# Kernel tuning notes

Hardware: AMD Instinct MI355X
Metric: run time of the kernel (lower is better)

The kernel has to match this reference:

```python
import jax, jax.numpy as jnp
import numpy as np

S_DIM, I_DIM, O_DIM = 1024, 2048, 1024
TOTAL = S_DIM + I_DIM + O_DIM  # 4096
INPUT_DIM, NUM_CLASSES, BATCH = 2048, 1000, 256


def setup_inputs() -> dict:
    key = jax.random.key(0)
    ks = jax.random.split(key, 6)
    x = jax.random.normal(ks[0], (BATCH, INPUT_DIM), dtype=jnp.float32)
    W = jax.random.normal(ks[1], (TOTAL, TOTAL), dtype=jnp.float32) * 0.02
    # torch Linear: weight [out, in], bias [out]
    in_w = jax.random.normal(ks[2], (S_DIM, INPUT_DIM), dtype=jnp.float32) * (1.0 / np.sqrt(INPUT_DIM))
    in_b = jax.random.normal(ks[3], (S_DIM,), dtype=jnp.float32) * 0.01
    out_w = jax.random.normal(ks[4], (NUM_CLASSES, O_DIM), dtype=jnp.float32) * (1.0 / np.sqrt(O_DIM))
    out_b = jax.random.normal(ks[5], (NUM_CLASSES,), dtype=jnp.float32) * 0.01
    return {"x": x, "W": W, "in_w": in_w, "in_b": in_b, "out_w": out_w, "out_b": out_b, "time_steps": 10}


def reference(x, W, in_w, in_b, out_w, out_b, time_steps):
    B = x.shape[0]
    S, I, O = S_DIM, I_DIM, O_DIM
    # slice effective W into 9 sub-blocks (use_lora=False -> W_eff = W)
    W_ss, W_sr, W_so = W[:S, :S], W[:S, S:S + I], W[:S, S + I:]
    W_rs, W_rr, W_ro = W[S:S + I, :S], W[S:S + I, S:S + I], W[S:S + I, S + I:]
    W_os, W_or, W_oo = W[S + I:, :S], W[S + I:, S:S + I], W[S + I:, S + I:]

    E = x @ in_w.T + in_b  # [B, S]
    gate = (jnp.arange(time_steps) % 5 == 0).astype(x.dtype)  # E injected when t%5==0

    init = (jnp.zeros((B, S), x.dtype), jnp.zeros((B, I), x.dtype), jnp.zeros((B, O), x.dtype))

    def step(carry, g):
        Ss, Is, Os = carry
        S_next = jax.nn.relu(Ss @ W_ss + g * E + Is @ W_rs + Os @ W_os)
        I_next = jax.nn.relu(Is @ W_rr + Ss @ W_sr + Os @ W_or)
        O_next = jax.nn.relu(Os @ W_oo + Is @ W_ro + Ss @ W_so)
        return (S_next, I_next, O_next), None

    (Ss, Is, Os), _ = jax.lax.scan(step, init, gate)
    return Os @ out_w.T + out_b  # [B, num_classes]
```

## Files before the change

### kernel.cpp

```cpp
#include <hip/hip_runtime.h>


typedef __bf16 bf16x8 __attribute__((ext_vector_type(8)));
typedef float  f32x16 __attribute__((ext_vector_type(16)));

#define TOTAL   4096
#define BATCH   256
#define INDIM   2048
#define SDIM    1024
#define NCLS    1000

__device__ inline f32x16 zero16() {
    f32x16 v;
#pragma unroll
    for (int i = 0; i < 16; ++i) v[i] = 0.f;
    return v;
}

__global__ __launch_bounds__(256) void k_transW_swz(const float* __restrict__ W,
                                                    __bf16* __restrict__ WT) {
    __shared__ float t[64][65];
    const int n0 = blockIdx.x * 64;
    const int k0 = blockIdx.y * 64;
    const int x = threadIdx.x & 63;
    const int y = threadIdx.x >> 6;
#pragma unroll
    for (int r = y; r < 64; r += 4)
        t[r][x] = W[(size_t)(k0 + r) * TOTAL + (n0 + x)];
    __syncthreads();
#pragma unroll
    for (int s = threadIdx.x; s < 512; s += 256) {
        const int frag = s >> 6;
        const int lane = s & 63;
        const int lrt = frag >> 2;
        const int lkc = frag & 3;
        const int r_local = lrt * 32 + (lane & 31);
        const int c_local = lkc * 16 + (lane >> 5) * 8;
        alignas(16) __bf16 v[8];
#pragma unroll
        for (int j = 0; j < 8; ++j) v[j] = (__bf16)t[c_local + j][r_local];
        const size_t fragG = (size_t)((n0 >> 5) + lrt) * (TOTAL / 16) + ((k0 >> 4) + lkc);
        *(ulonglong2*)(WT + fragG * 512 + lane * 8) = *(const ulonglong2*)v;
    }
}

__global__ __launch_bounds__(256) void k_swz(const float* __restrict__ in,
                                             __bf16* __restrict__ out,
                                             int C, int Rvalid) {
    const int t = blockIdx.x * blockDim.x + threadIdx.x;
    const int lane = t & 63;
    const int frag = t >> 6;
    const int kcN = C >> 4;
    const int rt = frag / kcN;
    const int kc = frag - rt * kcN;
    const int r = rt * 32 + (lane & 31);
    const int c = kc * 16 + (lane >> 5) * 8;
    alignas(16) __bf16 v[8];
    if (r < Rvalid) {
        const float* p = in + (size_t)r * C + c;
#pragma unroll
        for (int j = 0; j < 8; ++j) v[j] = (__bf16)p[j];
    } else {
#pragma unroll
        for (int j = 0; j < 8; ++j) v[j] = (__bf16)0.f;
    }
    *(ulonglong2*)(out + (size_t)t * 8) = *(const ulonglong2*)v;
}

__global__ __launch_bounds__(512, 4) void k_gemm_E(const __bf16* __restrict__ xt,
                                                   const __bf16* __restrict__ iwt,
                                                   const float* __restrict__ in_b,
                                                   float* __restrict__ E,
                                                   __bf16* __restrict__ h0) {
    __shared__ float red[8][1024];
    const int wave = threadIdx.x >> 6;
    const int lane = threadIdx.x & 63;
    const int mt = blockIdx.x >> 5;
    const int nt = blockIdx.x & 31;
    const int m0 = mt * 32, n0 = nt * 32;
    const int kc0 = wave * 16;
    const bf16x8* Ap = (const bf16x8*)xt  + ((size_t)mt * (INDIM / 16) + kc0) * 64 + lane;
    const bf16x8* Bp = (const bf16x8*)iwt + ((size_t)nt * (INDIM / 16) + kc0) * 64 + lane;
    f32x16 acc = zero16();
#pragma unroll 4
    for (int i = 0; i < 16; ++i) {
        bf16x8 a = Ap[i * 64];
        bf16x8 b = Bp[i * 64];
        acc = __builtin_amdgcn_mfma_f32_32x32x16_bf16(a, b, acc, 0, 0, 0);
    }
#pragma unroll
    for (int r = 0; r < 16; ++r) {
        int row = (r & 3) + 8 * (r >> 2) + 4 * (lane >> 5);
        red[wave][row * 32 + (lane & 31)] = acc[r];
    }
    __syncthreads();
    const int e0 = threadIdx.x * 2;
    float sx = 0.f, sy = 0.f;
#pragma unroll
    for (int w = 0; w < 8; ++w) {
        float2 v = *(const float2*)&red[w][e0];
        sx += v.x; sy += v.y;
    }
    const int row = e0 >> 5, col = e0 & 31;
    const int m = m0 + row, n = n0 + col;
    float v0 = sx + in_b[n], v1 = sy + in_b[n + 1];
    E[m * SDIM + n]     = v0;
    E[m * SDIM + n + 1] = v1;
    __bf16 o[2];
    o[0] = (__bf16)fmaxf(v0, 0.f);
    o[1] = (__bf16)fmaxf(v1, 0.f);
    const size_t frag = (size_t)(m >> 5) * (TOTAL / 16) + (n >> 4);
    const int lh = (m & 31) + 32 * ((n >> 3) & 1);
    *(uint*)(h0 + frag * 512 + lh * 8 + (n & 7)) = *(const uint*)o;
}

__global__ __launch_bounds__(512, 2) void k_step(const __bf16* __restrict__ h,
                                                 const __bf16* __restrict__ WT,
                                                 const float* __restrict__ E,
                                                 const int gate,
                                                 __bf16* __restrict__ hn,
                                                 const int chunks) {
    __shared__ float buf[4][4096];
    const int wave = threadIdx.x >> 6;
    const int lane = threadIdx.x & 63;
    const int mt = blockIdx.x >> 6;
    const int nt = blockIdx.x & 63;
    const int per = chunks >> 3;
    const int kc0 = wave * per;

    const bf16x8* A0 = (const bf16x8*)h  + ((size_t)(mt * 2) * (TOTAL / 16) + kc0) * 64 + lane;
    const bf16x8* A1 = A0 + (size_t)(TOTAL / 16) * 64;
    const bf16x8* B0 = (const bf16x8*)WT + ((size_t)(nt * 2) * (TOTAL / 16) + kc0) * 64 + lane;
    const bf16x8* B1 = B0 + (size_t)(TOTAL / 16) * 64;

    f32x16 ac0 = zero16(), ac1 = zero16(), ac2 = zero16(), ac3 = zero16();
#pragma unroll 4
    for (int i = 0; i < per; ++i) {
        const int off = i * 64;
        bf16x8 a0 = A0[off];
        bf16x8 a1 = A1[off];
        bf16x8 b0 = B0[off];
        bf16x8 b1 = B1[off];
        ac0 = __builtin_amdgcn_mfma_f32_32x32x16_bf16(a0, b0, ac0, 0, 0, 0);
        ac1 = __builtin_amdgcn_mfma_f32_32x32x16_bf16(a0, b1, ac1, 0, 0, 0);
        ac2 = __builtin_amdgcn_mfma_f32_32x32x16_bf16(a1, b0, ac2, 0, 0, 0);
        ac3 = __builtin_amdgcn_mfma_f32_32x32x16_bf16(a1, b1, ac3, 0, 0, 0);
    }

    float* accp[4];
    f32x16 accs[4] = {ac0, ac1, ac2, ac3};
    if (wave >= 4) {
        float* b = buf[wave - 4];
#pragma unroll
        for (int c = 0; c < 4; ++c)
#pragma unroll
            for (int r = 0; r < 16; ++r)
                b[(c * 16 + r) * 64 + lane] = accs[c][r];
    }
    __syncthreads();
    if (wave < 4) {
        float* b = buf[wave];
#pragma unroll
        for (int c = 0; c < 4; ++c)
#pragma unroll
            for (int r = 0; r < 16; ++r) {
                const int idx = (c * 16 + r) * 64 + lane;
                b[idx] += accs[c][r];
            }
    }
    __syncthreads();

    const int t = threadIdx.x;
    const int c = t >> 7;
    const int r = (t >> 3) & 15;
    const int l0 = (t & 7) * 8;
    const int base = (c * 16 + r) * 64 + l0;
    float4 s0 = {0.f, 0.f, 0.f, 0.f}, s1 = {0.f, 0.f, 0.f, 0.f};
#pragma unroll
    for (int w = 0; w < 4; ++w) {
        const float4* p = (const float4*)&buf[w][base];
        float4 v0 = p[0], v1 = p[1];
        s0.x += v0.x; s0.y += v0.y; s0.z += v0.z; s0.w += v0.w;
        s1.x += v1.x; s1.y += v1.y; s1.z += v1.z; s1.w += v1.w;
    }
    float v[8] = {s0.x, s0.y, s0.z, s0.w, s1.x, s1.y, s1.z, s1.w};
    const int ih = c >> 1, jh = c & 1;
    const int row = ih * 32 + (r & 3) + 8 * (r >> 2) + 4 * (l0 >> 5);
    const int col0 = jh * 32 + (l0 & 31);
    const int m = mt * 64 + row;
    const int n0g = nt * 64 + col0;
    if (gate && n0g < SDIM) {
        const float* Ep = E + m * SDIM + n0g;
#pragma unroll
        for (int j = 0; j < 8; ++j) v[j] += Ep[j];
    }
    alignas(16) __bf16 o[8];
#pragma unroll
    for (int j = 0; j < 8; ++j) o[j] = (__bf16)fmaxf(v[j], 0.f);
    const size_t frag = (size_t)(m >> 5) * (TOTAL / 16) + (n0g >> 4);
    const int lh = (m & 31) + 32 * ((n0g >> 3) & 1);
    *(ulonglong2*)(hn + frag * 512 + lh * 8) = *(const ulonglong2*)o;
    (void)accp;
}

__global__ __launch_bounds__(512, 4) void k_out(const __bf16* __restrict__ h,
                                                const __bf16* __restrict__ owt,
                                                const float* __restrict__ out_b,
                                                float* __restrict__ out) {
    __shared__ float red[8][1024];
    const int wave = threadIdx.x >> 6;
    const int lane = threadIdx.x & 63;
    const int mt = blockIdx.x >> 5;
    const int ct = blockIdx.x & 31;
    const int m0 = mt * 32, c0 = ct * 32;
    const int kcA0 = (3072 / 16) + wave * 8;
    const int kcB0 = wave * 8;
    const bf16x8* Ap = (const bf16x8*)h   + ((size_t)mt * (TOTAL / 16) + kcA0) * 64 + lane;
    const bf16x8* Bp = (const bf16x8*)owt + ((size_t)ct * (1024 / 16) + kcB0) * 64 + lane;
    f32x16 acc = zero16();
#pragma unroll
    for (int i = 0; i < 8; ++i) {
        bf16x8 a = Ap[i * 64];
        bf16x8 b = Bp[i * 64];
        acc = __builtin_amdgcn_mfma_f32_32x32x16_bf16(a, b, acc, 0, 0, 0);
    }
#pragma unroll
    for (int r = 0; r < 16; ++r) {
        int row = (r & 3) + 8 * (r >> 2) + 4 * (lane >> 5);
        red[wave][row * 32 + (lane & 31)] = acc[r];
    }
    __syncthreads();
    const int e0 = threadIdx.x * 2;
    float sx = 0.f, sy = 0.f;
#pragma unroll
    for (int w = 0; w < 8; ++w) {
        float2 v = *(const float2*)&red[w][e0];
        sx += v.x; sy += v.y;
    }
    const int row = e0 >> 5, col = e0 & 31;
    const int m = m0 + row;
    const int n = c0 + col;
    if (n < NCLS)     out[m * NCLS + n]     = sx + out_b[n];
    if (n + 1 < NCLS) out[m * NCLS + n + 1] = sy + out_b[n + 1];
}

extern "C" void kernel_launch(void* const* d_in, const int* in_sizes, int n_in,
                              void* d_out, int out_size, void* d_ws, size_t ws_size,
                              hipStream_t stream) {
    const float* x     = (const float*)d_in[0];
    const float* W     = (const float*)d_in[1];
    const float* in_w  = (const float*)d_in[2];
    const float* in_b  = (const float*)d_in[3];
    const float* out_w = (const float*)d_in[4];
    const float* out_b = (const float*)d_in[5];
    float* out = (float*)d_out;

    char* ws = (char*)d_ws;
    __bf16* WT  = (__bf16*)(ws + 0);
    __bf16* XT  = (__bf16*)(ws + 33554432);
    __bf16* IWT = (__bf16*)(ws + 34603008);
    __bf16* OWT = (__bf16*)(ws + 38797312);
    float*  Ebuf= (float*)(ws + 40894464);
    __bf16* H0  = (__bf16*)(ws + 41943040);
    __bf16* H1  = (__bf16*)(ws + 44040192);

    k_transW_swz<<<dim3(64, 64), 256, 0, stream>>>(W, WT);
    k_swz<<<256,  256, 0, stream>>>(x,     XT,  INDIM, BATCH);
    k_swz<<<1024, 256, 0, stream>>>(in_w,  IWT, INDIM, SDIM);
    k_swz<<<512,  256, 0, stream>>>(out_w, OWT, 1024,  NCLS);

    k_gemm_E<<<256, 512, 0, stream>>>(XT, IWT, in_b, Ebuf, H0);

    const __bf16* hs = H0;
    __bf16* hd = H1;
    for (int t = 1; t < 10; ++t) {
        const int chunks = (t == 1) ? (SDIM / 16) : (TOTAL / 16);
        k_step<<<256, 512, 0, stream>>>(hs, WT, Ebuf, (t % 5 == 0) ? 1 : 0, hd, chunks);
        const __bf16* tmp = hs; hs = hd; hd = (__bf16*)tmp;
    }

    k_out<<<256, 512, 0, stream>>>(hs, OWT, out_b, out);
}
```

Measured before the change: 278.1 us.

## Fuse all stages into one cooperative persistent kernel with grid syncs

Replaces the 15 separate launches (weight swizzle, E GEMM, nine recurrent steps, output GEMM) with a single cooperative kernel of 256 blocks that uses grid.sync between phases. The W transpose is overlapped with the E GEMM, and the step inner loop is software-pipelined to prefetch the next fragments. This removes per-launch overhead and inter-kernel gaps, at the cost of grid-wide barrier latency and a fixed block count that must all be co-resident.

```diff
diff --git a/kernel.cpp b/kernel.cpp
--- a/kernel.cpp
+++ b/kernel.cpp
@@ -1,14 +1,25 @@
 #include <hip/hip_runtime.h>
+#include <hip/hip_cooperative_groups.h>
+
+namespace cg = cooperative_groups;
 
 
 typedef __bf16 bf16x8 __attribute__((ext_vector_type(8)));
 typedef float  f32x16 __attribute__((ext_vector_type(16)));
 
-#define TOTAL   4096
-#define BATCH   256
-#define INDIM   2048
-#define SDIM    1024
-#define NCLS    1000
+#define TOTAL 4096
+#define BATCH 256
+#define INDIM 2048
+#define SDIM  1024
+#define NCLS  1000
+
+#define MFMA(a, b, c) __builtin_amdgcn_mfma_f32_32x32x16_bf16((a), (b), (c), 0, 0, 0)
+
+union ShMem {
+    float trans[64][65];
+    float red8[8][1024];
+    float buf4[4][4096];
+};
 
 __device__ inline f32x16 zero16() {
     f32x16 v;
@@ -17,231 +28,244 @@
     return v;
 }
 
-__global__ __launch_bounds__(256) void k_transW_swz(const float* __restrict__ W,
-                                                    __bf16* __restrict__ WT) {
-    __shared__ float t[64][65];
-    const int n0 = blockIdx.x * 64;
-    const int k0 = blockIdx.y * 64;
-    const int x = threadIdx.x & 63;
-    const int y = threadIdx.x >> 6;
-#pragma unroll
-    for (int r = y; r < 64; r += 4)
-        t[r][x] = W[(size_t)(k0 + r) * TOTAL + (n0 + x)];
-    __syncthreads();
-#pragma unroll
-    for (int s = threadIdx.x; s < 512; s += 256) {
-        const int frag = s >> 6;
-        const int lane = s & 63;
-        const int lrt = frag >> 2;
-        const int lkc = frag & 3;
-        const int r_local = lrt * 32 + (lane & 31);
-        const int c_local = lkc * 16 + (lane >> 5) * 8;
+__device__ inline void swz_dev(const float* __restrict__ in, __bf16* __restrict__ out,
+                               int C, int Rvalid, int nslots, int gtid, int gstride) {
+    for (int t = gtid; t < nslots; t += gstride) {
+        const int lane = t & 63;
+        const int frag = t >> 6;
+        const int kcN = C >> 4;
+        const int rt = frag / kcN;
+        const int kc = frag - rt * kcN;
+        const int r = rt * 32 + (lane & 31);
+        const int c = kc * 16 + (lane >> 5) * 8;
         alignas(16) __bf16 v[8];
-#pragma unroll
-        for (int j = 0; j < 8; ++j) v[j] = (__bf16)t[c_local + j][r_local];
-        const size_t fragG = (size_t)((n0 >> 5) + lrt) * (TOTAL / 16) + ((k0 >> 4) + lkc);
-        *(ulonglong2*)(WT + fragG * 512 + lane * 8) = *(const ulonglong2*)v;
-    }
-}
-
-__global__ __launch_bounds__(256) void k_swz(const float* __restrict__ in,
-                                             __bf16* __restrict__ out,
-                                             int C, int Rvalid) {
-    const int t = blockIdx.x * blockDim.x + threadIdx.x;
-    const int lane = t & 63;
-    const int frag = t >> 6;
-    const int kcN = C >> 4;
-    const int rt = frag / kcN;
-    const int kc = frag - rt * kcN;
-    const int r = rt * 32 + (lane & 31);
-    const int c = kc * 16 + (lane >> 5) * 8;
-    alignas(16) __bf16 v[8];
-    if (r < Rvalid) {
-        const float* p = in + (size_t)r * C + c;
-#pragma unroll
-        for (int j = 0; j < 8; ++j) v[j] = (__bf16)p[j];
-    } else {
-#pragma unroll
-        for (int j = 0; j < 8; ++j) v[j] = (__bf16)0.f;
-    }
-    *(ulonglong2*)(out + (size_t)t * 8) = *(const ulonglong2*)v;
-}
-
-__global__ __launch_bounds__(512, 4) void k_gemm_E(const __bf16* __restrict__ xt,
-                                                   const __bf16* __restrict__ iwt,
-                                                   const float* __restrict__ in_b,
-                                                   float* __restrict__ E,
-                                                   __bf16* __restrict__ h0) {
-    __shared__ float red[8][1024];
-    const int wave = threadIdx.x >> 6;
-    const int lane = threadIdx.x & 63;
-    const int mt = blockIdx.x >> 5;
-    const int nt = blockIdx.x & 31;
-    const int m0 = mt * 32, n0 = nt * 32;
-    const int kc0 = wave * 16;
-    const bf16x8* Ap = (const bf16x8*)xt  + ((size_t)mt * (INDIM / 16) + kc0) * 64 + lane;
-    const bf16x8* Bp = (const bf16x8*)iwt + ((size_t)nt * (INDIM / 16) + kc0) * 64 + lane;
-    f32x16 acc = zero16();
+        if (r < Rvalid) {
+            const float* p = in + (size_t)r * C + c;
+#pragma unroll
+            for (int j = 0; j < 8; ++j) v[j] = (__bf16)p[j];
+        } else {
+#pragma unroll
+            for (int j = 0; j < 8; ++j) v[j] = (__bf16)0.f;
+        }
+        *(ulonglong2*)(out + (size_t)t * 8) = *(const ulonglong2*)v;
+    }
+}
+
+template <int PER>
+__device__ inline void step_core(const bf16x8* __restrict__ A0, const bf16x8* __restrict__ A1,
+                                 const bf16x8* __restrict__ B0, const bf16x8* __restrict__ B1,
+                                 f32x16& ac0, f32x16& ac1, f32x16& ac2, f32x16& ac3) {
+    bf16x8 a0 = A0[0], a1 = A1[0], b0 = B0[0], b1 = B1[0];
 #pragma unroll 4
-    for (int i = 0; i < 16; ++i) {
-        bf16x8 a = Ap[i * 64];
-        bf16x8 b = Bp[i * 64];
-        acc = __builtin_amdgcn_mfma_f32_32x32x16_bf16(a, b, acc, 0, 0, 0);
-    }
-#pragma unroll
-    for (int r = 0; r < 16; ++r) {
-        int row = (r & 3) + 8 * (r >> 2) + 4 * (lane >> 5);
-        red[wave][row * 32 + (lane & 31)] = acc[r];
-    }
-    __syncthreads();
-    const int e0 = threadIdx.x * 2;
-    float sx = 0.f, sy = 0.f;
-#pragma unroll
-    for (int w = 0; w < 8; ++w) {
-        float2 v = *(const float2*)&red[w][e0];
-        sx += v.x; sy += v.y;
-    }
-    const int row = e0 >> 5, col = e0 & 31;
-    const int m = m0 + row, n = n0 + col;
-    float v0 = sx + in_b[n], v1 = sy + in_b[n + 1];
-    E[m * SDIM + n]     = v0;
-    E[m * SDIM + n + 1] = v1;
-    __bf16 o[2];
-    o[0] = (__bf16)fmaxf(v0, 0.f);
-    o[1] = (__bf16)fmaxf(v1, 0.f);
-    const size_t frag = (size_t)(m >> 5) * (TOTAL / 16) + (n >> 4);
-    const int lh = (m & 31) + 32 * ((n >> 3) & 1);
-    *(uint*)(h0 + frag * 512 + lh * 8 + (n & 7)) = *(const uint*)o;
-}
-
-__global__ __launch_bounds__(512, 2) void k_step(const __bf16* __restrict__ h,
-                                                 const __bf16* __restrict__ WT,
-                                                 const float* __restrict__ E,
-                                                 const int gate,
-                                                 __bf16* __restrict__ hn,
-                                                 const int chunks) {
-    __shared__ float buf[4][4096];
-    const int wave = threadIdx.x >> 6;
-    const int lane = threadIdx.x & 63;
-    const int mt = blockIdx.x >> 6;
-    const int nt = blockIdx.x & 63;
-    const int per = chunks >> 3;
-    const int kc0 = wave * per;
-
-    const bf16x8* A0 = (const bf16x8*)h  + ((size_t)(mt * 2) * (TOTAL / 16) + kc0) * 64 + lane;
-    const bf16x8* A1 = A0 + (size_t)(TOTAL / 16) * 64;
-    const bf16x8* B0 = (const bf16x8*)WT + ((size_t)(nt * 2) * (TOTAL / 16) + kc0) * 64 + lane;
-    const bf16x8* B1 = B0 + (size_t)(TOTAL / 16) * 64;
-
-    f32x16 ac0 = zero16(), ac1 = zero16(), ac2 = zero16(), ac3 = zero16();
+    for (int i = 0; i < PER - 1; ++i) {
+        const int off = (i + 1) * 64;
+        bf16x8 na0 = A0[off], na1 = A1[off], nb0 = B0[off], nb1 = B1[off];
+        ac0 = MFMA(a0, b0, ac0);
+        ac1 = MFMA(a0, b1, ac1);
+        ac2 = MFMA(a1, b0, ac2);
+        ac3 = MFMA(a1, b1, ac3);
+        a0 = na0; a1 = na1; b0 = nb0; b1 = nb1;
+    }
+    ac0 = MFMA(a0, b0, ac0);
+    ac1 = MFMA(a0, b1, ac1);
+    ac2 = MFMA(a1, b0, ac2);
+    ac3 = MFMA(a1, b1, ac3);
+}
+
+__global__ __launch_bounds__(512, 2) void k_mega(
+    const float* __restrict__ x, const float* __restrict__ W,
+    const float* __restrict__ in_w, const float* __restrict__ in_b,
+    const float* __restrict__ out_w, const float* __restrict__ out_b,
+    float* __restrict__ out, void* __restrict__ wsv) {
+    __shared__ ShMem sh;
+    cg::grid_group grid = cg::this_grid();
+
+    char* ws = (char*)wsv;
+    __bf16* WT   = (__bf16*)(ws + 0);
+    __bf16* XT   = (__bf16*)(ws + 33554432);
+    __bf16* IWT  = (__bf16*)(ws + 34603008);
+    __bf16* OWT  = (__bf16*)(ws + 38797312);
+    float*  Ebuf = (float*)(ws + 40894464);
+    __bf16* H0   = (__bf16*)(ws + 41943040);
+    __bf16* H1   = (__bf16*)(ws + 44040192);
+
+    const int tid = threadIdx.x;
+    const int bid = blockIdx.x;
+    const int gtid = bid * 512 + tid;
+    const int gstride = 256 * 512;
+    const int wave = tid >> 6;
+    const int lane = tid & 63;
+
+    swz_dev(x, XT, INDIM, BATCH, (BATCH / 32) * (INDIM / 16) * 64, gtid, gstride);
+    swz_dev(in_w, IWT, INDIM, SDIM, (SDIM / 32) * (INDIM / 16) * 64, gtid, gstride);
+    grid.sync();
+
+    {
+        const int mt = bid >> 5, nt = bid & 31;
+        const int m0 = mt * 32, n0 = nt * 32;
+        const int kc0 = wave * 16;
+        const bf16x8* Ap = (const bf16x8*)XT + ((size_t)mt * (INDIM / 16) + kc0) * 64 + lane;
+        const bf16x8* Bp = (const bf16x8*)IWT + ((size_t)nt * (INDIM / 16) + kc0) * 64 + lane;
+        f32x16 acc = zero16();
 #pragma unroll 4
-    for (int i = 0; i < per; ++i) {
-        const int off = i * 64;
-        bf16x8 a0 = A0[off];
-        bf16x8 a1 = A1[off];
-        bf16x8 b0 = B0[off];
-        bf16x8 b1 = B1[off];
-        ac0 = __builtin_amdgcn_mfma_f32_32x32x16_bf16(a0, b0, ac0, 0, 0, 0);
-        ac1 = __builtin_amdgcn_mfma_f32_32x32x16_bf16(a0, b1, ac1, 0, 0, 0);
-        ac2 = __builtin_amdgcn_mfma_f32_32x32x16_bf16(a1, b0, ac2, 0, 0, 0);
-        ac3 = __builtin_amdgcn_mfma_f32_32x32x16_bf16(a1, b1, ac3, 0, 0, 0);
-    }
-
-    float* accp[4];
-    f32x16 accs[4] = {ac0, ac1, ac2, ac3};
-    if (wave >= 4) {
-        float* b = buf[wave - 4];
-#pragma unroll
-        for (int c = 0; c < 4; ++c)
-#pragma unroll
-            for (int r = 0; r < 16; ++r)
-                b[(c * 16 + r) * 64 + lane] = accs[c][r];
-    }
-    __syncthreads();
-    if (wave < 4) {
-        float* b = buf[wave];
-#pragma unroll
-        for (int c = 0; c < 4; ++c)
-#pragma unroll
-            for (int r = 0; r < 16; ++r) {
-                const int idx = (c * 16 + r) * 64 + lane;
-                b[idx] += accs[c][r];
-            }
-    }
-    __syncthreads();
-
-    const int t = threadIdx.x;
-    const int c = t >> 7;
-    const int r = (t >> 3) & 15;
-    const int l0 = (t & 7) * 8;
-    const int base = (c * 16 + r) * 64 + l0;
-    float4 s0 = {0.f, 0.f, 0.f, 0.f}, s1 = {0.f, 0.f, 0.f, 0.f};
-#pragma unroll
-    for (int w = 0; w < 4; ++w) {
-        const float4* p = (const float4*)&buf[w][base];
-        float4 v0 = p[0], v1 = p[1];
-        s0.x += v0.x; s0.y += v0.y; s0.z += v0.z; s0.w += v0.w;
-        s1.x += v1.x; s1.y += v1.y; s1.z += v1.z; s1.w += v1.w;
-    }
-    float v[8] = {s0.x, s0.y, s0.z, s0.w, s1.x, s1.y, s1.z, s1.w};
-    const int ih = c >> 1, jh = c & 1;
-    const int row = ih * 32 + (r & 3) + 8 * (r >> 2) + 4 * (l0 >> 5);
-    const int col0 = jh * 32 + (l0 & 31);
-    const int m = mt * 64 + row;
-    const int n0g = nt * 64 + col0;
-    if (gate && n0g < SDIM) {
-        const float* Ep = E + m * SDIM + n0g;
-#pragma unroll
-        for (int j = 0; j < 8; ++j) v[j] += Ep[j];
-    }
-    alignas(16) __bf16 o[8];
-#pragma unroll
-    for (int j = 0; j < 8; ++j) o[j] = (__bf16)fmaxf(v[j], 0.f);
-    const size_t frag = (size_t)(m >> 5) * (TOTAL / 16) + (n0g >> 4);
-    const int lh = (m & 31) + 32 * ((n0g >> 3) & 1);
-    *(ulonglong2*)(hn + frag * 512 + lh * 8) = *(const ulonglong2*)o;
-    (void)accp;
-}
-
-__global__ __launch_bounds__(512, 4) void k_out(const __bf16* __restrict__ h,
-                                                const __bf16* __restrict__ owt,
-                                                const float* __restrict__ out_b,
-                                                float* __restrict__ out) {
-    __shared__ float red[8][1024];
-    const int wave = threadIdx.x >> 6;
-    const int lane = threadIdx.x & 63;
-    const int mt = blockIdx.x >> 5;
-    const int ct = blockIdx.x & 31;
-    const int m0 = mt * 32, c0 = ct * 32;
-    const int kcA0 = (3072 / 16) + wave * 8;
-    const int kcB0 = wave * 8;
-    const bf16x8* Ap = (const bf16x8*)h   + ((size_t)mt * (TOTAL / 16) + kcA0) * 64 + lane;
-    const bf16x8* Bp = (const bf16x8*)owt + ((size_t)ct * (1024 / 16) + kcB0) * 64 + lane;
-    f32x16 acc = zero16();
-#pragma unroll
-    for (int i = 0; i < 8; ++i) {
-        bf16x8 a = Ap[i * 64];
-        bf16x8 b = Bp[i * 64];
-        acc = __builtin_amdgcn_mfma_f32_32x32x16_bf16(a, b, acc, 0, 0, 0);
-    }
-#pragma unroll
-    for (int r = 0; r < 16; ++r) {
-        int row = (r & 3) + 8 * (r >> 2) + 4 * (lane >> 5);
-        red[wave][row * 32 + (lane & 31)] = acc[r];
-    }
-    __syncthreads();
-    const int e0 = threadIdx.x * 2;
-    float sx = 0.f, sy = 0.f;
-#pragma unroll
-    for (int w = 0; w < 8; ++w) {
-        float2 v = *(const float2*)&red[w][e0];
-        sx += v.x; sy += v.y;
-    }
-    const int row = e0 >> 5, col = e0 & 31;
-    const int m = m0 + row;
-    const int n = c0 + col;
-    if (n < NCLS)     out[m * NCLS + n]     = sx + out_b[n];
-    if (n + 1 < NCLS) out[m * NCLS + n + 1] = sy + out_b[n + 1];
+        for (int i = 0; i < 16; ++i)
+            acc = MFMA(Ap[i * 64], Bp[i * 64], acc);
+#pragma unroll
+        for (int r = 0; r < 16; ++r) {
+            int row = (r & 3) + 8 * (r >> 2) + 4 * (lane >> 5);
+            sh.red8[wave][row * 32 + (lane & 31)] = acc[r];
+        }
+        __syncthreads();
+        const int e0 = tid * 2;
+        float sx = 0.f, sy = 0.f;
+#pragma unroll
+        for (int w = 0; w < 8; ++w) {
+            float2 v = *(const float2*)&sh.red8[w][e0];
+            sx += v.x; sy += v.y;
+        }
+        const int row = e0 >> 5, col = e0 & 31;
+        const int m = m0 + row, n = n0 + col;
+        float v0 = sx + in_b[n], v1 = sy + in_b[n + 1];
+        Ebuf[m * SDIM + n] = v0;
+        Ebuf[m * SDIM + n + 1] = v1;
+        __bf16 o[2];
+        o[0] = (__bf16)fmaxf(v0, 0.f);
+        o[1] = (__bf16)fmaxf(v1, 0.f);
+        const size_t frag = (size_t)(m >> 5) * (TOTAL / 16) + (n >> 4);
+        const int lh = (m & 31) + 32 * ((n >> 3) & 1);
+        *(uint*)(H0 + frag * 512 + lh * 8 + (n & 7)) = *(const uint*)o;
+        __syncthreads();
+    }
+    {
+        const int x64 = tid & 63;
+        const int y8 = tid >> 6;
+        for (int it = 0; it < 16; ++it) {
+            const int T = bid * 16 + it;
+            const int n0 = (T & 63) * 64;
+            const int k0 = (T >> 6) * 64;
+#pragma unroll
+            for (int r = y8; r < 64; r += 8)
+                sh.trans[r][x64] = W[(size_t)(k0 + r) * TOTAL + n0 + x64];
+            __syncthreads();
+            const int frag = tid >> 6;
+            const int lrt = frag >> 2, lkc = frag & 3;
+            const int r_local = lrt * 32 + (x64 & 31);
+            const int c_local = lkc * 16 + (x64 >> 5) * 8;
+            alignas(16) __bf16 v[8];
+#pragma unroll
+            for (int j = 0; j < 8; ++j) v[j] = (__bf16)sh.trans[c_local + j][r_local];
+            const size_t fragG = (size_t)((n0 >> 5) + lrt) * (TOTAL / 16) + (k0 >> 4) + lkc;
+            *(ulonglong2*)(WT + fragG * 512 + x64 * 8) = *(const ulonglong2*)v;
+            __syncthreads();
+        }
+        swz_dev(out_w, OWT, 1024, NCLS, (1024 / 32) * (1024 / 16) * 64, gtid, gstride);
+    }
+    grid.sync();
+
+    const __bf16* hs = H0;
+    __bf16* hd = H1;
+    const int mtS = bid >> 6;
+    const int ntS = bid & 63;
+    for (int t = 1; t < 10; ++t) {
+        const int chunks = (t == 1) ? (SDIM / 16) : (TOTAL / 16);
+        const int per = chunks >> 3;
+        const int kc0 = wave * per;
+        const int gate = (t == 5);
+
+        const bf16x8* A0 = (const bf16x8*)hs + ((size_t)(mtS * 2) * (TOTAL / 16) + kc0) * 64 + lane;
+        const bf16x8* A1 = A0 + (size_t)(TOTAL / 16) * 64;
+        const bf16x8* B0 = (const bf16x8*)WT + ((size_t)(ntS * 2) * (TOTAL / 16) + kc0) * 64 + lane;
+        const bf16x8* B1 = B0 + (size_t)(TOTAL / 16) * 64;
+        f32x16 ac0 = zero16(), ac1 = zero16(), ac2 = zero16(), ac3 = zero16();
+        if (t == 1) step_core<8>(A0, A1, B0, B1, ac0, ac1, ac2, ac3);
+        else        step_core<32>(A0, A1, B0, B1, ac0, ac1, ac2, ac3);
+
+        f32x16 accs[4] = {ac0, ac1, ac2, ac3};
+        if (wave >= 4) {
+            float* b = sh.buf4[wave - 4];
+#pragma unroll
+            for (int c = 0; c < 4; ++c)
+#pragma unroll
+                for (int r = 0; r < 16; ++r)
+                    b[(c * 16 + r) * 64 + lane] = accs[c][r];
+        }
+        __syncthreads();
+        if (wave < 4) {
+            float* b = sh.buf4[wave];
+#pragma unroll
+            for (int c = 0; c < 4; ++c)
+#pragma unroll
+                for (int r = 0; r < 16; ++r) {
+                    const int idx = (c * 16 + r) * 64 + lane;
+                    b[idx] += accs[c][r];
+                }
+        }
+        __syncthreads();
+
+        const int c = tid >> 7;
+        const int r = (tid >> 3) & 15;
+        const int l0 = (tid & 7) * 8;
+        const int base = (c * 16 + r) * 64 + l0;
+        float4 s0 = {0.f, 0.f, 0.f, 0.f}, s1 = {0.f, 0.f, 0.f, 0.f};
+#pragma unroll
+        for (int w = 0; w < 4; ++w) {
+            const float4* p = (const float4*)&sh.buf4[w][base];
+            float4 v0 = p[0], v1 = p[1];
+            s0.x += v0.x; s0.y += v0.y; s0.z += v0.z; s0.w += v0.w;
+            s1.x += v1.x; s1.y += v1.y; s1.z += v1.z; s1.w += v1.w;
+        }
+        float v[8] = {s0.x, s0.y, s0.z, s0.w, s1.x, s1.y, s1.z, s1.w};
+        const int ih = c >> 1, jh = c & 1;
+        const int row = ih * 32 + (r & 3) + 8 * (r >> 2) + 4 * (l0 >> 5);
+        const int col0 = jh * 32 + (l0 & 31);
+        const int m = mtS * 64 + row;
+        const int n0g = ntS * 64 + col0;
+        if (gate && n0g < SDIM) {
+            const float* Ep = Ebuf + m * SDIM + n0g;
+#pragma unroll
+            for (int j = 0; j < 8; ++j) v[j] += Ep[j];
+        }
+        alignas(16) __bf16 o[8];
+#pragma unroll
+        for (int j = 0; j < 8; ++j) o[j] = (__bf16)fmaxf(v[j], 0.f);
+        const size_t frag = (size_t)(m >> 5) * (TOTAL / 16) + (n0g >> 4);
+        const int lh = (m & 31) + 32 * ((n0g >> 3) & 1);
+        *(ulonglong2*)(hd + frag * 512 + lh * 8) = *(const ulonglong2*)o;
+
+        grid.sync();
+        const __bf16* tmp = hs; hs = hd; hd = (__bf16*)tmp;
+    }
+
+    {
+        const int mt = bid >> 5, ct = bid & 31;
+        const int m0 = mt * 32, c0 = ct * 32;
+        const int kcA0 = (3072 / 16) + wave * 8;
+        const int kcB0 = wave * 8;
+        const bf16x8* Ap = (const bf16x8*)hs + ((size_t)mt * (TOTAL / 16) + kcA0) * 64 + lane;
+        const bf16x8* Bp = (const bf16x8*)OWT + ((size_t)ct * (1024 / 16) + kcB0) * 64 + lane;
+        f32x16 acc = zero16();
+#pragma unroll
+        for (int i = 0; i < 8; ++i)
+            acc = MFMA(Ap[i * 64], Bp[i * 64], acc);
+#pragma unroll
+        for (int r = 0; r < 16; ++r) {
+            int row = (r & 3) + 8 * (r >> 2) + 4 * (lane >> 5);
+            sh.red8[wave][row * 32 + (lane & 31)] = acc[r];
+        }
+        __syncthreads();
+        const int e0 = tid * 2;
+        float sx = 0.f, sy = 0.f;
+#pragma unroll
+        for (int w = 0; w < 8; ++w) {
+            float2 v = *(const float2*)&sh.red8[w][e0];
+            sx += v.x; sy += v.y;
+        }
+        const int row = e0 >> 5, col = e0 & 31;
+        const int m = m0 + row;
+        const int n = c0 + col;
+        if (n < NCLS)     out[m * NCLS + n] = sx + out_b[n];
+        if (n + 1 < NCLS) out[m * NCLS + n + 1] = sy + out_b[n + 1];
+    }
 }
 
 extern "C" void kernel_launch(void* const* d_in, const int* in_sizes, int n_in,
@@ -254,30 +278,9 @@
     const float* out_w = (const float*)d_in[4];
     const float* out_b = (const float*)d_in[5];
     float* out = (float*)d_out;
-
-    char* ws = (char*)d_ws;
-    __bf16* WT  = (__bf16*)(ws + 0);
-    __bf16* XT  = (__bf16*)(ws + 33554432);
-    __bf16* IWT = (__bf16*)(ws + 34603008);
-    __bf16* OWT = (__bf16*)(ws + 38797312);
-    float*  Ebuf= (float*)(ws + 40894464);
-    __bf16* H0  = (__bf16*)(ws + 41943040);
-    __bf16* H1  = (__bf16*)(ws + 44040192);
-
-    k_transW_swz<<<dim3(64, 64), 256, 0, stream>>>(W, WT);
-    k_swz<<<256,  256, 0, stream>>>(x,     XT,  INDIM, BATCH);
-    k_swz<<<1024, 256, 0, stream>>>(in_w,  IWT, INDIM, SDIM);
-    k_swz<<<512,  256, 0, stream>>>(out_w, OWT, 1024,  NCLS);
-
-    k_gemm_E<<<256, 512, 0, stream>>>(XT, IWT, in_b, Ebuf, H0);
-
-    const __bf16* hs = H0;
-    __bf16* hd = H1;
-    for (int t = 1; t < 10; ++t) {
-        const int chunks = (t == 1) ? (SDIM / 16) : (TOTAL / 16);
-        k_step<<<256, 512, 0, stream>>>(hs, WT, Ebuf, (t % 5 == 0) ? 1 : 0, hd, chunks);
-        const __bf16* tmp = hs; hs = hd; hd = (__bf16*)tmp;
-    }
-
-    k_out<<<256, 512, 0, stream>>>(hs, OWT, out_b, out);
-}
+    void* wsv = d_ws;
+
+    void* args[] = {(void*)&x, (void*)&W, (void*)&in_w, (void*)&in_b,
+                    (void*)&out_w, (void*)&out_b, (void*)&out, (void*)&wsv};
+    hipLaunchCooperativeKernel((const void*)k_mega, dim3(256), dim3(512), args, 0, stream);
+}
```

Result: slower. 651.5 us (+134.3%).
